# Performance work log

Measured on AMD Instinct MI355X. Metric: run time of the kernel, lower is better.

Reference implementation:

```python
import jax, jax.numpy as jnp
import numpy as np

WS = 7      # window_size
NH = 12     # num_heads
SHIFT = 3   # shift_size

def _rel_pos_index(ws):
    coords = np.stack(np.meshgrid(np.arange(ws), np.arange(ws), indexing='ij')).reshape(2, -1)
    rel = (coords[:, :, None] - coords[:, None, :]).transpose(1, 2, 0)  # [N,N,2]
    rel[..., 0] += ws - 1
    rel[..., 1] += ws - 1
    rel[..., 0] *= 2 * ws - 1
    return jnp.asarray(rel.sum(-1))  # [N,N] int

REL_IDX = _rel_pos_index(WS)

def _ln(x, g, b, eps=1e-5):
    m = x.mean(-1, keepdims=True)
    v = ((x - m) ** 2).mean(-1, keepdims=True)
    return (x - m) / jnp.sqrt(v + eps) * g + b

def setup_inputs() -> dict:
    key = jax.random.key(0)
    ks = jax.random.split(key, 10)
    B, H, W, C = 16, 56, 56, 384
    Dff = 4 * C
    s = 0.02
    return {
        'x': jax.random.normal(ks[0], (B, H * W, C), jnp.float32),
        'norm1_g': jnp.ones((C,), jnp.float32),
        'norm1_b': jnp.zeros((C,), jnp.float32),
        'qkv_w': jax.random.normal(ks[1], (3 * C, C), jnp.float32) * s,
        'qkv_b': jax.random.normal(ks[2], (3 * C,), jnp.float32) * s,
        'proj_w': jax.random.normal(ks[3], (C, C), jnp.float32) * s,
        'proj_b': jax.random.normal(ks[4], (C,), jnp.float32) * s,
        'rpb_table': jax.random.normal(ks[5], ((2 * WS - 1) ** 2, NH), jnp.float32) * s,
        'norm2_g': jnp.ones((C,), jnp.float32),
        'norm2_b': jnp.zeros((C,), jnp.float32),
        'mlp_w1': jax.random.normal(ks[6], (Dff, C), jnp.float32) * s,
        'mlp_b1': jax.random.normal(ks[7], (Dff,), jnp.float32) * s,
        'mlp_w2': jax.random.normal(ks[8], (C, Dff), jnp.float32) * s,
        'mlp_b2': jax.random.normal(ks[9], (C,), jnp.float32) * s,
        'H': H,
        'W': W,
    }

def reference(x, norm1_g, norm1_b, qkv_w, qkv_b, proj_w, proj_b, rpb_table,
              norm2_g, norm2_b, mlp_w1, mlp_b1, mlp_w2, mlp_b2, H, W):
    B, L, C = x.shape
    # --- norm1 + shift + window partition ---
    h = _ln(x, norm1_g, norm1_b).reshape(B, H, W, C)
    h = jnp.roll(h, (-SHIFT, -SHIFT), axis=(1, 2))
    nh, nw = H // WS, W // WS
    xw = h.reshape(B, nh, WS, nw, WS, C).transpose(0, 1, 3, 2, 4, 5).reshape(-1, WS * WS, C)
    # --- window attention with relative position bias ---
    Bw, N, _ = xw.shape
    hd = C // NH
    qkv = (xw @ qkv_w.T + qkv_b).reshape(Bw, N, 3, NH, hd).transpose(2, 0, 3, 1, 4)
    q, k, v = qkv[0] * (hd ** -0.5), qkv[1], qkv[2]  # [Bw,NH,N,hd]
    attn = jnp.einsum('bhnd,bhmd->bhnm', q, k)
    bias = rpb_table[REL_IDX.reshape(-1)].reshape(N, N, NH).transpose(2, 0, 1)  # [NH,N,N]
    attn = jax.nn.softmax(attn + bias[None], axis=-1)
    o = jnp.einsum('bhnm,bhmd->bhnd', attn, v).transpose(0, 2, 1, 3).reshape(Bw, N, C)
    o = o @ proj_w.T + proj_b
    # --- window reverse + unshift + residual ---
    o = o.reshape(B, nh, nw, WS, WS, C).transpose(0, 1, 3, 2, 4, 5).reshape(B, H, W, C)
    o = jnp.roll(o, (SHIFT, SHIFT), axis=(1, 2)).reshape(B, L, C)
    x = x + o
    # --- MLP ---
    h = _ln(x, norm2_g, norm2_b)
    h = jax.nn.gelu(h @ mlp_w1.T + mlp_b1, approximate=False) @ mlp_w2.T + mlp_b2
    return x + h
```

## Files before the change

### kernel.cpp

```cpp
#include <hip/hip_runtime.h>

typedef unsigned short ushort_t;
typedef unsigned int uint32;
typedef __attribute__((ext_vector_type(8))) short short8;
typedef __attribute__((ext_vector_type(4))) float floatx4;

static __device__ __forceinline__ ushort_t f2bf(float f) {
    union { float f; unsigned int u; } c; c.f = f;
    unsigned int u = c.u;
    return (ushort_t)((u + 0x7FFFu + ((u >> 16) & 1u)) >> 16);
}

static __device__ __forceinline__ int swz_off(int row, int slot16) {
    return row * 64 + (((slot16 ^ (row & 7)) & 7) << 3);
}

__global__ __launch_bounds__(256) void cvt_weights(
    const float* __restrict__ w0, const float* __restrict__ w1,
    const float* __restrict__ w2, const float* __restrict__ w3,
    ushort_t* __restrict__ o0, ushort_t* __restrict__ o1,
    ushort_t* __restrict__ o2, ushort_t* __restrict__ o3)
{
    int i = blockIdx.x * 256 + threadIdx.x;
    if (i < 442368) o0[i] = f2bf(w0[i]);
    if (i < 147456) o1[i] = f2bf(w1[i]);
    if (i < 589824) o2[i] = f2bf(w2[i]);
    if (i < 589824) o3[i] = f2bf(w3[i]);
}

__global__ __launch_bounds__(256) void build_bias(
    const float* __restrict__ rpb, float* __restrict__ biasM)
{
    int idx = blockIdx.x * 256 + threadIdx.x;
    int h = idx >> 12, q = (idx >> 6) & 63, j = idx & 63;
    float v = 0.f;
    if (q < 49 && j < 49) {
        int pi = q / 7, pj = q - pi * 7;
        int qi = j / 7, qj = j - qi * 7;
        v = rpb[((pi - qi + 6) * 13 + (pj - qj + 6)) * 12 + h];
    }
    biasM[idx] = v;
}

template<bool WPART>
__global__ __launch_bounds__(256) void ln_kernel(
    const float* __restrict__ x, const float* __restrict__ g,
    const float* __restrict__ b, ushort_t* __restrict__ out)
{
    int wave = threadIdx.x >> 6, lane = threadIdx.x & 63;
    int tkn = blockIdx.x * 4 + wave;
    const float* src;
    if (WPART) {
        int w = tkn / 49, n = tkn - w * 49;
        int bb = w >> 6, wrem = w & 63;
        int wi = wrem >> 3, wj = wrem & 7;
        int pi = n / 7, pj = n - pi * 7;
        int si = wi * 7 + pi + 3; if (si >= 56) si -= 56;
        int sj = wj * 7 + pj + 3; if (sj >= 56) sj -= 56;
        src = x + ((size_t)bb * 3136 + si * 56 + sj) * 384;
    } else {
        src = x + (size_t)tkn * 384;
    }
    float v[6];
    float s = 0.f, sq = 0.f;
#pragma unroll
    for (int it = 0; it < 3; ++it) {
        float2 t = *(const float2*)(src + it * 128 + lane * 2);
        v[it * 2] = t.x; v[it * 2 + 1] = t.y;
        s += t.x + t.y; sq += t.x * t.x + t.y * t.y;
    }
#pragma unroll
    for (int off = 32; off; off >>= 1) {
        s += __shfl_xor(s, off, 64);
        sq += __shfl_xor(sq, off, 64);
    }
    float mean = s * (1.f / 384.f);
    float rstd = rsqrtf(sq * (1.f / 384.f) - mean * mean + 1e-5f);
    ushort_t* dst = out + (size_t)tkn * 384;
#pragma unroll
    for (int it = 0; it < 3; ++it) {
        int c = it * 128 + lane * 2;
        float2 gg = *(const float2*)(g + c);
        float2 bb2 = *(const float2*)(b + c);
        float y0 = (v[it * 2] - mean) * rstd * gg.x + bb2.x;
        float y1 = (v[it * 2 + 1] - mean) * rstd * gg.y + bb2.y;
        uint32 pack = ((uint32)f2bf(y0)) | (((uint32)f2bf(y1)) << 16);
        *(uint32*)(dst + c) = pack;
    }
}

template<int EPI>
__global__ __launch_bounds__(256, 2) void gemm_bt(
    const ushort_t* __restrict__ A, const ushort_t* __restrict__ Bw,
    const float* __restrict__ bias, void* __restrict__ out,
    const float* __restrict__ resid, int M, int N, int K)
{
    __shared__ __align__(16) ushort_t As[2][128 * 64];
    __shared__ __align__(16) ushort_t Bs[2][128 * 64];
    int tid = threadIdx.x;

    int nwg = gridDim.x;
    int orig = blockIdx.x;
    int xcd = orig & 7, lid = orig >> 3;
    int q8 = nwg >> 3, r8 = nwg & 7;
    int swz = (xcd < r8 ? xcd * (q8 + 1) : r8 * (q8 + 1) + (xcd - r8) * q8) + lid;
    int bnT = N >> 7;
    int bm = swz / bnT, bn = swz - bm * bnT;

    int wv = tid >> 6, lane = tid & 63;
    int wr = wv >> 1, wc = wv & 1;
    int quad = lane >> 4, l15 = lane & 15;
    int r0 = tid >> 3, s0 = tid & 7;

    floatx4 acc[4][4];
#pragma unroll
    for (int mi = 0; mi < 4; ++mi)
#pragma unroll
        for (int ni = 0; ni < 4; ++ni)
            acc[mi][ni] = (floatx4){0.f, 0.f, 0.f, 0.f};

    const ushort_t* Ar0 = A + (size_t)(bm * 128 + r0) * K + s0 * 8;
    const ushort_t* Ar1 = Ar0 + (size_t)32 * K;
    const ushort_t* Ar2 = Ar0 + (size_t)64 * K;
    const ushort_t* Ar3 = Ar0 + (size_t)96 * K;
    const ushort_t* Br0 = Bw + (size_t)(bn * 128 + r0) * K + s0 * 8;
    const ushort_t* Br1 = Br0 + (size_t)32 * K;
    const ushort_t* Br2 = Br0 + (size_t)64 * K;
    const ushort_t* Br3 = Br0 + (size_t)96 * K;

    int w0 = swz_off(r0, s0), w1 = swz_off(r0 + 32, s0);
    int w2 = swz_off(r0 + 64, s0), w3 = swz_off(r0 + 96, s0);

#define GLOAD(a0,a1,a2,a3,b0,b1,b2,b3,k0) \
    a0 = *(const uint4*)(Ar0 + (k0)); a1 = *(const uint4*)(Ar1 + (k0)); \
    a2 = *(const uint4*)(Ar2 + (k0)); a3 = *(const uint4*)(Ar3 + (k0)); \
    b0 = *(const uint4*)(Br0 + (k0)); b1 = *(const uint4*)(Br1 + (k0)); \
    b2 = *(const uint4*)(Br2 + (k0)); b3 = *(const uint4*)(Br3 + (k0));

#define SWRITE(buf,a0,a1,a2,a3,b0,b1,b2,b3) \
    *(uint4*)&As[buf][w0] = a0; *(uint4*)&As[buf][w1] = a1; \
    *(uint4*)&As[buf][w2] = a2; *(uint4*)&As[buf][w3] = a3; \
    *(uint4*)&Bs[buf][w0] = b0; *(uint4*)&Bs[buf][w1] = b1; \
    *(uint4*)&Bs[buf][w2] = b2; *(uint4*)&Bs[buf][w3] = b3;

#define COMPUTE(buf) \
    _Pragma("unroll") \
    for (int kk = 0; kk < 64; kk += 32) { \
        short8 af[4], bfr[4]; \
        _Pragma("unroll") \
        for (int mi = 0; mi < 4; ++mi) \
            af[mi] = *(const short8*)&As[buf][swz_off(wr * 64 + mi * 16 + l15, (kk >> 3) + quad)]; \
        _Pragma("unroll") \
        for (int ni = 0; ni < 4; ++ni) \
            bfr[ni] = *(const short8*)&Bs[buf][swz_off(wc * 64 + ni * 16 + l15, (kk >> 3) + quad)]; \
        _Pragma("unroll") \
        for (int mi = 0; mi < 4; ++mi) \
            _Pragma("unroll") \
            for (int ni = 0; ni < 4; ++ni) \
                acc[mi][ni] = __builtin_amdgcn_mfma_f32_16x16x32_bf16( \
                    af[mi], bfr[ni], acc[mi][ni], 0, 0, 0); \
    }

    int nK = K >> 6;
    uint4 pa0, pa1, pa2, pa3, pb0, pb1, pb2, pb3;
    uint4 qa0, qa1, qa2, qa3, qb0, qb1, qb2, qb3;

    GLOAD(pa0, pa1, pa2, pa3, pb0, pb1, pb2, pb3, 0);
    GLOAD(qa0, qa1, qa2, qa3, qb0, qb1, qb2, qb3, 64);
    SWRITE(0, pa0, pa1, pa2, pa3, pb0, pb1, pb2, pb3);
    if (nK > 2) { GLOAD(pa0, pa1, pa2, pa3, pb0, pb1, pb2, pb3, 128); }
    __syncthreads();

    for (int kt = 0; kt < nK; kt += 2) {
        COMPUTE(0);
        SWRITE(1, qa0, qa1, qa2, qa3, qb0, qb1, qb2, qb3);
        if (kt + 3 < nK) { int k0 = (kt + 3) << 6; GLOAD(qa0, qa1, qa2, qa3, qb0, qb1, qb2, qb3, k0); }
        __syncthreads();
        COMPUTE(1);
        if (kt + 2 < nK) {
            SWRITE(0, pa0, pa1, pa2, pa3, pb0, pb1, pb2, pb3);
            if (kt + 4 < nK) { int k0 = (kt + 4) << 6; GLOAD(pa0, pa1, pa2, pa3, pb0, pb1, pb2, pb3, k0); }
            __syncthreads();
        }
    }
#undef GLOAD
#undef SWRITE
#undef COMPUTE

#pragma unroll
    for (int mi = 0; mi < 4; ++mi) {
#pragma unroll
        for (int ni = 0; ni < 4; ++ni) {
            int gn = bn * 128 + wc * 64 + ni * 16 + l15;
            float bv = bias[gn];
#pragma unroll
            for (int r = 0; r < 4; ++r) {
                int gm = bm * 128 + wr * 64 + mi * 16 + quad * 4 + r;
                float v = acc[mi][ni][r] + bv;
                if (EPI == 0) {
                    if (gn < 384) v *= 0.17677669529663689f;
                    ((ushort_t*)out)[(size_t)gm * N + gn] = f2bf(v);
                } else if (EPI == 1) {
                    v = 0.5f * v * (1.f + erff(v * 0.70710678118654752f));
                    ((ushort_t*)out)[(size_t)gm * N + gn] = f2bf(v);
                } else if (EPI == 2) {
                    int wdx = gm / 49, n = gm - wdx * 49;
                    int b = wdx >> 6, wrem = wdx & 63;
                    int wi = wrem >> 3, wj = wrem & 7;
                    int pi = n / 7, pj = n - pi * 7;
                    int i = wi * 7 + pi + 3; if (i >= 56) i -= 56;
                    int j = wj * 7 + pj + 3; if (j >= 56) j -= 56;
                    size_t dst = ((size_t)b * 3136 + i * 56 + j) * 384 + gn;
                    ((float*)out)[dst] = resid[dst] + v;
                } else {
                    size_t dst = (size_t)gm * 384 + gn;
                    ((float*)out)[dst] = resid[dst] + v;
                }
            }
        }
    }
}

__global__ __launch_bounds__(256) void attn_kernel(
    const ushort_t* __restrict__ qkv,
    const float* __restrict__ biasM,
    ushort_t* __restrict__ O)
{
    __shared__ __align__(16) ushort_t Pl[4][64][72];
    __shared__ __align__(16) ushort_t Vt[4][32][72];
    int wave = threadIdx.x >> 6;
    int lane = threadIdx.x & 63;
    int id = blockIdx.x * 4 + wave;
    int w = id / 12, h = id % 12;
    int quad = lane >> 4, l15 = lane & 15;
    ushort_t (*P)[72] = Pl[wave];
    ushort_t (*V)[72] = Vt[wave];

    for (int i = lane; i < 32 * 16; i += 64) {
        int d = i >> 4, j = 48 + (i & 15);
        V[d][j] = 0;
    }
    for (int idx = lane; idx < 49 * 4; idx += 64) {
        int j = idx >> 2, seg = idx & 3;
        const ushort_t* src = qkv + (size_t)(w * 49 + j) * 1152 + 768 + h * 32 + seg * 8;
        uint4 u = *(const uint4*)src;
        const ushort_t* tmp = (const ushort_t*)&u;
#pragma unroll
        for (int t = 0; t < 8; ++t) V[seg * 8 + t][j] = tmp[t];
    }

    short8 aQ[4], bK[4];
#pragma unroll
    for (int t = 0; t < 4; ++t) {
        int row = t * 16 + l15; if (row > 48) row = 48;
        aQ[t] = *(const short8*)(qkv + (size_t)(w * 49 + row) * 1152 + h * 32 + quad * 8);
        bK[t] = *(const short8*)(qkv + (size_t)(w * 49 + row) * 1152 + 384 + h * 32 + quad * 8);
    }
    floatx4 S[4][4];
    floatx4 z4 = (floatx4){0.f, 0.f, 0.f, 0.f};
#pragma unroll
    for (int mt = 0; mt < 4; ++mt)
#pragma unroll
        for (int nt = 0; nt < 4; ++nt)
            S[mt][nt] = __builtin_amdgcn_mfma_f32_16x16x32_bf16(aQ[mt], bK[nt], z4, 0, 0, 0);

    const float* bh = biasM + h * 4096;
#pragma unroll
    for (int mt = 0; mt < 4; ++mt) {
#pragma unroll
        for (int r = 0; r < 4; ++r) {
            int q = mt * 16 + quad * 4 + r;
            float mx = -1e30f;
#pragma unroll
            for (int nt = 0; nt < 4; ++nt) {
                int j = nt * 16 + l15;
                float sv = S[mt][nt][r] + bh[q * 64 + j];
                if (j >= 49) sv = -1e30f;
                S[mt][nt][r] = sv;
                mx = fmaxf(mx, sv);
            }
#pragma unroll
            for (int off = 1; off < 16; off <<= 1) mx = fmaxf(mx, __shfl_xor(mx, off, 64));
            float sum = 0.f;
#pragma unroll
            for (int nt = 0; nt < 4; ++nt) {
                int j = nt * 16 + l15;
                float p = __expf(S[mt][nt][r] - mx);
                if (j >= 49) p = 0.f;
                S[mt][nt][r] = p;
                sum += p;
            }
#pragma unroll
            for (int off = 1; off < 16; off <<= 1) sum += __shfl_xor(sum, off, 64);
            float inv = 1.f / sum;
#pragma unroll
            for (int nt = 0; nt < 4; ++nt) {
                int j = nt * 16 + l15;
                P[q][j] = f2bf(S[mt][nt][r] * inv);
            }
        }
    }
    __syncthreads();

    short8 aV[2][2];
#pragma unroll
    for (int mt = 0; mt < 2; ++mt)
#pragma unroll
        for (int kt = 0; kt < 2; ++kt)
            aV[mt][kt] = *(const short8*)&V[mt * 16 + l15][kt * 32 + quad * 8];
    floatx4 Oc[2][4];
#pragma unroll
    for (int mt = 0; mt < 2; ++mt)
#pragma unroll
        for (int nt = 0; nt < 4; ++nt)
            Oc[mt][nt] = z4;
#pragma unroll
    for (int nt = 0; nt < 4; ++nt) {
#pragma unroll
        for (int kt = 0; kt < 2; ++kt) {
            short8 bP = *(const short8*)&P[nt * 16 + l15][kt * 32 + quad * 8];
#pragma unroll
            for (int mt = 0; mt < 2; ++mt)
                Oc[mt][nt] = __builtin_amdgcn_mfma_f32_16x16x32_bf16(
                    aV[mt][kt], bP, Oc[mt][nt], 0, 0, 0);
        }
    }
#pragma unroll
    for (int nt = 0; nt < 4; ++nt) {
        int query = nt * 16 + l15;
        if (query < 49) {
#pragma unroll
            for (int mt = 0; mt < 2; ++mt) {
                ushort4 pk;
                pk.x = f2bf(Oc[mt][nt][0]);
                pk.y = f2bf(Oc[mt][nt][1]);
                pk.z = f2bf(Oc[mt][nt][2]);
                pk.w = f2bf(Oc[mt][nt][3]);
                *(ushort4*)(O + (size_t)(w * 49 + query) * 384 + h * 32 + mt * 16 + quad * 4) = pk;
            }
        }
    }
}

extern "C" void kernel_launch(void* const* d_in, const int* in_sizes, int n_in,
                              void* d_out, int out_size, void* d_ws, size_t ws_size,
                              hipStream_t stream) {
    const float* x      = (const float*)d_in[0];
    const float* n1g    = (const float*)d_in[1];
    const float* n1b    = (const float*)d_in[2];
    const float* qkv_w  = (const float*)d_in[3];
    const float* qkv_b  = (const float*)d_in[4];
    const float* proj_w = (const float*)d_in[5];
    const float* proj_b = (const float*)d_in[6];
    const float* rpb    = (const float*)d_in[7];
    const float* n2g    = (const float*)d_in[8];
    const float* n2b    = (const float*)d_in[9];
    const float* w1     = (const float*)d_in[10];
    const float* b1     = (const float*)d_in[11];
    const float* w2     = (const float*)d_in[12];
    const float* b2     = (const float*)d_in[13];
    float* out = (float*)d_out;
    char* ws = (char*)d_ws;

    ushort_t* qkvbuf = (ushort_t*)ws;
    ushort_t* bufA   = (ushort_t*)(ws + 115605504);
    ushort_t* wq     = (ushort_t*)(ws + 154140672);
    ushort_t* wp     = wq + 442368;
    ushort_t* wm1    = wp + 147456;
    ushort_t* wm2    = wm1 + 589824;
    float* biasM     = (float*)(ws + 154140672 + 3538944);

    cvt_weights<<<2304, 256, 0, stream>>>(qkv_w, proj_w, w1, w2, wq, wp, wm1, wm2);
    build_bias<<<192, 256, 0, stream>>>(rpb, biasM);

    ln_kernel<true><<<12544, 256, 0, stream>>>(x, n1g, n1b, bufA);
    gemm_bt<0><<<3528, 256, 0, stream>>>(bufA, wq, qkv_b, qkvbuf, nullptr, 50176, 1152, 384);
    attn_kernel<<<3072, 256, 0, stream>>>(qkvbuf, biasM, bufA);
    gemm_bt<2><<<1176, 256, 0, stream>>>(bufA, wp, proj_b, out, x, 50176, 384, 384);
    ln_kernel<false><<<12544, 256, 0, stream>>>(out, n2g, n2b, bufA);
    for (int half = 0; half < 2; ++half) {
        size_t mo = (size_t)half * 25088;
        gemm_bt<1><<<2352, 256, 0, stream>>>(bufA + mo * 384, wm1, b1, qkvbuf, nullptr, 25088, 1536, 384);
        gemm_bt<3><<<588, 256, 0, stream>>>(qkvbuf, wm2, b2, out + mo * 384, out + mo * 384, 25088, 384, 1536);
    }
}
```

Measured before the change: 579.1 us.

## Load V directly into registers, transpose bias table, swizzle P in LDS

The attention kernel no longer stages V through shared memory. It gathers the V fragments directly from global memory into MFMA registers and replaces the __syncthreads with a wave-local LDS wait. The relative-position bias is stored transposed so each lane can fetch four query values with one float4 load. The P tile uses an XOR swizzle instead of padded rows to avoid bank conflicts. The proj epilogue hoists the window-reverse index math out of the column loop, but the per-element scalar global gathers of V may cost more than the old staged copy.

```diff
diff --git a/kernel.cpp b/kernel.cpp
--- a/kernel.cpp
+++ b/kernel.cpp
@@ -29,17 +29,17 @@
 }
 
 __global__ __launch_bounds__(256) void build_bias(
-    const float* __restrict__ rpb, float* __restrict__ biasM)
+    const float* __restrict__ rpb, float* __restrict__ biasT)
 {
     int idx = blockIdx.x * 256 + threadIdx.x;
-    int h = idx >> 12, q = (idx >> 6) & 63, j = idx & 63;
+    int h = idx >> 12, j = (idx >> 6) & 63, q = idx & 63;
     float v = 0.f;
     if (q < 49 && j < 49) {
         int pi = q / 7, pj = q - pi * 7;
         int qi = j / 7, qj = j - qi * 7;
         v = rpb[((pi - qi + 6) * 13 + (pj - qj + 6)) * 12 + h];
     }
-    biasM[idx] = v;
+    biasT[idx] = v;
 }
 
 template<bool WPART>
@@ -187,34 +187,50 @@
 #undef SWRITE
 #undef COMPUTE
 
-#pragma unroll
-    for (int mi = 0; mi < 4; ++mi) {
-#pragma unroll
-        for (int ni = 0; ni < 4; ++ni) {
-            int gn = bn * 128 + wc * 64 + ni * 16 + l15;
-            float bv = bias[gn];
+    if (EPI == 2) {
+        float bv4[4];
+#pragma unroll
+        for (int ni = 0; ni < 4; ++ni) bv4[ni] = bias[bn * 128 + wc * 64 + ni * 16 + l15];
+#pragma unroll
+        for (int mi = 0; mi < 4; ++mi) {
 #pragma unroll
             for (int r = 0; r < 4; ++r) {
                 int gm = bm * 128 + wr * 64 + mi * 16 + quad * 4 + r;
-                float v = acc[mi][ni][r] + bv;
-                if (EPI == 0) {
-                    if (gn < 384) v *= 0.17677669529663689f;
-                    ((ushort_t*)out)[(size_t)gm * N + gn] = f2bf(v);
-                } else if (EPI == 1) {
-                    v = 0.5f * v * (1.f + erff(v * 0.70710678118654752f));
-                    ((ushort_t*)out)[(size_t)gm * N + gn] = f2bf(v);
-                } else if (EPI == 2) {
-                    int wdx = gm / 49, n = gm - wdx * 49;
-                    int b = wdx >> 6, wrem = wdx & 63;
-                    int wi = wrem >> 3, wj = wrem & 7;
-                    int pi = n / 7, pj = n - pi * 7;
-                    int i = wi * 7 + pi + 3; if (i >= 56) i -= 56;
-                    int j = wj * 7 + pj + 3; if (j >= 56) j -= 56;
-                    size_t dst = ((size_t)b * 3136 + i * 56 + j) * 384 + gn;
-                    ((float*)out)[dst] = resid[dst] + v;
-                } else {
-                    size_t dst = (size_t)gm * 384 + gn;
-                    ((float*)out)[dst] = resid[dst] + v;
+                int wdx = gm / 49, n = gm - wdx * 49;
+                int b = wdx >> 6, wrem = wdx & 63;
+                int wi = wrem >> 3, wj = wrem & 7;
+                int pi = n / 7, pj = n - pi * 7;
+                int i = wi * 7 + pi + 3; if (i >= 56) i -= 56;
+                int j = wj * 7 + pj + 3; if (j >= 56) j -= 56;
+                size_t base = ((size_t)b * 3136 + i * 56 + j) * 384;
+#pragma unroll
+                for (int ni = 0; ni < 4; ++ni) {
+                    size_t dst = base + bn * 128 + wc * 64 + ni * 16 + l15;
+                    ((float*)out)[dst] = resid[dst] + acc[mi][ni][r] + bv4[ni];
+                }
+            }
+        }
+    } else {
+#pragma unroll
+        for (int mi = 0; mi < 4; ++mi) {
+#pragma unroll
+            for (int ni = 0; ni < 4; ++ni) {
+                int gn = bn * 128 + wc * 64 + ni * 16 + l15;
+                float bv = bias[gn];
+#pragma unroll
+                for (int r = 0; r < 4; ++r) {
+                    int gm = bm * 128 + wr * 64 + mi * 16 + quad * 4 + r;
+                    float v = acc[mi][ni][r] + bv;
+                    if (EPI == 0) {
+                        if (gn < 384) v *= 0.17677669529663689f;
+                        ((ushort_t*)out)[(size_t)gm * N + gn] = f2bf(v);
+                    } else if (EPI == 1) {
+                        v = 0.5f * v * (1.f + erff(v * 0.70710678118654752f));
+                        ((ushort_t*)out)[(size_t)gm * N + gn] = f2bf(v);
+                    } else {
+                        size_t dst = (size_t)gm * 384 + gn;
+                        ((float*)out)[dst] = resid[dst] + v;
+                    }
                 }
             }
         }
@@ -223,31 +239,16 @@
 
 __global__ __launch_bounds__(256) void attn_kernel(
     const ushort_t* __restrict__ qkv,
-    const float* __restrict__ biasM,
+    const float* __restrict__ biasT,
     ushort_t* __restrict__ O)
 {
-    __shared__ __align__(16) ushort_t Pl[4][64][72];
-    __shared__ __align__(16) ushort_t Vt[4][32][72];
+    __shared__ __align__(16) ushort_t Pl[4][64 * 64];
     int wave = threadIdx.x >> 6;
     int lane = threadIdx.x & 63;
     int id = blockIdx.x * 4 + wave;
     int w = id / 12, h = id % 12;
     int quad = lane >> 4, l15 = lane & 15;
-    ushort_t (*P)[72] = Pl[wave];
-    ushort_t (*V)[72] = Vt[wave];
-
-    for (int i = lane; i < 32 * 16; i += 64) {
-        int d = i >> 4, j = 48 + (i & 15);
-        V[d][j] = 0;
-    }
-    for (int idx = lane; idx < 49 * 4; idx += 64) {
-        int j = idx >> 2, seg = idx & 3;
-        const ushort_t* src = qkv + (size_t)(w * 49 + j) * 1152 + 768 + h * 32 + seg * 8;
-        uint4 u = *(const uint4*)src;
-        const ushort_t* tmp = (const ushort_t*)&u;
-#pragma unroll
-        for (int t = 0; t < 8; ++t) V[seg * 8 + t][j] = tmp[t];
-    }
+    ushort_t* P = Pl[wave];
 
     short8 aQ[4], bK[4];
 #pragma unroll
@@ -264,17 +265,36 @@
         for (int nt = 0; nt < 4; ++nt)
             S[mt][nt] = __builtin_amdgcn_mfma_f32_16x16x32_bf16(aQ[mt], bK[nt], z4, 0, 0, 0);
 
-    const float* bh = biasM + h * 4096;
+    short8 aV[2][2];
+#pragma unroll
+    for (int mt = 0; mt < 2; ++mt)
+#pragma unroll
+        for (int kt = 0; kt < 2; ++kt) {
+            short8 v;
+#pragma unroll
+            for (int t = 0; t < 8; ++t) {
+                int j = kt * 32 + quad * 8 + t; if (j > 48) j = 48;
+                v[t] = (short)qkv[(size_t)(w * 49 + j) * 1152 + 768 + h * 32 + mt * 16 + l15];
+            }
+            aV[mt][kt] = v;
+        }
+
+    const float* bT = biasT + h * 4096;
 #pragma unroll
     for (int mt = 0; mt < 4; ++mt) {
+        float4 bq[4];
+#pragma unroll
+        for (int nt = 0; nt < 4; ++nt)
+            bq[nt] = *(const float4*)(bT + (nt * 16 + l15) * 64 + mt * 16 + quad * 4);
 #pragma unroll
         for (int r = 0; r < 4; ++r) {
             int q = mt * 16 + quad * 4 + r;
+            int key = (q ^ (q >> 3)) & 7;
             float mx = -1e30f;
 #pragma unroll
             for (int nt = 0; nt < 4; ++nt) {
                 int j = nt * 16 + l15;
-                float sv = S[mt][nt][r] + bh[q * 64 + j];
+                float sv = S[mt][nt][r] + ((const float*)&bq[nt])[r];
                 if (j >= 49) sv = -1e30f;
                 S[mt][nt][r] = sv;
                 mx = fmaxf(mx, sv);
@@ -296,18 +316,13 @@
 #pragma unroll
             for (int nt = 0; nt < 4; ++nt) {
                 int j = nt * 16 + l15;
-                P[q][j] = f2bf(S[mt][nt][r] * inv);
-            }
-        }
-    }
-    __syncthreads();
-
-    short8 aV[2][2];
-#pragma unroll
-    for (int mt = 0; mt < 2; ++mt)
-#pragma unroll
-        for (int kt = 0; kt < 2; ++kt)
-            aV[mt][kt] = *(const short8*)&V[mt * 16 + l15][kt * 32 + quad * 8];
+                P[q * 64 + (((j >> 3) ^ key) << 3) + (j & 7)] = f2bf(S[mt][nt][r] * inv);
+            }
+        }
+    }
+    asm volatile("s_waitcnt lgkmcnt(0)" ::: "memory");
+    __builtin_amdgcn_sched_barrier(0);
+
     floatx4 Oc[2][4];
 #pragma unroll
     for (int mt = 0; mt < 2; ++mt)
@@ -316,9 +331,12 @@
             Oc[mt][nt] = z4;
 #pragma unroll
     for (int nt = 0; nt < 4; ++nt) {
+        int query = nt * 16 + l15;
+        int key = (query ^ (query >> 3)) & 7;
 #pragma unroll
         for (int kt = 0; kt < 2; ++kt) {
-            short8 bP = *(const short8*)&P[nt * 16 + l15][kt * 32 + quad * 8];
+            int slot = ((kt * 4 + quad) ^ key) & 7;
+            short8 bP = *(const short8*)&P[query * 64 + slot * 8];
 #pragma unroll
             for (int mt = 0; mt < 2; ++mt)
                 Oc[mt][nt] = __builtin_amdgcn_mfma_f32_16x16x32_bf16(
@@ -368,14 +386,14 @@
     ushort_t* wp     = wq + 442368;
     ushort_t* wm1    = wp + 147456;
     ushort_t* wm2    = wm1 + 589824;
-    float* biasM     = (float*)(ws + 154140672 + 3538944);
+    float* biasT     = (float*)(ws + 154140672 + 3538944);
 
     cvt_weights<<<2304, 256, 0, stream>>>(qkv_w, proj_w, w1, w2, wq, wp, wm1, wm2);
-    build_bias<<<192, 256, 0, stream>>>(rpb, biasM);
+    build_bias<<<192, 256, 0, stream>>>(rpb, biasT);
 
     ln_kernel<true><<<12544, 256, 0, stream>>>(x, n1g, n1b, bufA);
     gemm_bt<0><<<3528, 256, 0, stream>>>(bufA, wq, qkv_b, qkvbuf, nullptr, 50176, 1152, 384);
-    attn_kernel<<<3072, 256, 0, stream>>>(qkvbuf, biasM, bufA);
+    attn_kernel<<<3072, 256, 0, stream>>>(qkvbuf, biasT, bufA);
     gemm_bt<2><<<1176, 256, 0, stream>>>(bufA, wp, proj_b, out, x, 50176, 384, 384);
     ln_kernel<false><<<12544, 256, 0, stream>>>(out, n2g, n2b, bufA);
     for (int half = 0; half < 2; ++half) {
```

Measured after the change: 562.3 us. -2.9%, faster.
